# Kernel optimization log

Hardware: AMD Instinct MI355X
Metric: run time of the kernel (lower is better)

The kernel has to match this reference:

```python
import jax, jax.numpy as jnp
import numpy as np

B = 8192      # batch
D = 512       # ode state dim = 4*h_dim
U = 100       # ode net hidden units
K_STEPS = 20  # opt.ode1_step
EPS = 0.01    # opt.ode2_eps


def setup_inputs() -> dict:
    key = jax.random.key(0)
    ks = jax.random.split(key, 12)
    std = 0.1  # init_network_weights std
    return {
        "y0": jax.random.normal(ks[0], (B, D), jnp.float32),
        "t_seq": jax.random.uniform(ks[1], (B, 2), dtype=jnp.float32),
        "W1": std * jax.random.normal(ks[2], (U, D), jnp.float32),
        "b1": jnp.zeros((U,), jnp.float32),
        "W2": std * jax.random.normal(ks[3], (U, U), jnp.float32),
        "b2": jnp.zeros((U,), jnp.float32),
        "W3": std * jax.random.normal(ks[4], (D, U), jnp.float32),
        "b3": jnp.zeros((D,), jnp.float32),
        "b_phi_zt": jax.random.normal(ks[5], (B, 1), jnp.float32),
        # derivative of Nonpositive net is <= 0; log(-b' + 0.01) requires b' < 0.01
        "b_phi_zt_deriv": -jax.random.uniform(ks[6], (B, 1), dtype=jnp.float32),
        "s_phi_zt": jax.random.normal(ks[7], (B, 1), jnp.float32),
        "s_phi_zt_deriv": jax.random.uniform(ks[8], (B, 1), dtype=jnp.float32),
        "k": K_STEPS,
    }


def _ode_net(y, W1, b1, W2, b2, W3, b3):
    # create_net(D, D, n_layers=1, n_units=U): Linear->Tanh->Linear->Tanh->Linear
    h = jnp.tanh(y @ W1.T + b1)
    h = jnp.tanh(h @ W2.T + b2)
    return h @ W3.T + b3


def _forward(y0, t_seq, W1, b1, W2, b2, W3, b3,
             b_phi_zt, b_phi_zt_deriv, s_phi_zt, s_phi_zt_deriv, k):
    # ---- DiffeqSolver: k fixed Euler steps, gradient net ignores t ----
    dt = (t_seq[:, 1:2] - t_seq[:, 0:1]) / k  # [B,1]

    def euler_step(yi, _):
        yi = yi + _ode_net(yi, W1, b1, W2, b2, W3, b3) * dt
        return yi, None

    y_final, _ = jax.lax.scan(euler_step, y0, None, length=k)

    # ---- DiffeqSolver_KL: y_t = y0 + eps * cumsum(g(m_t)); y0 = 0 ----
    const = 0.01
    Kv = s_phi_zt + jnp.log(-b_phi_zt_deriv + const) - jnp.log(s_phi_zt_deriv + const)  # [B,1]
    T = int(round(1.0 / EPS)) - 1  # steps t = 1 .. int(1/eps)-1
    ms = (-1.0 + EPS * jnp.arange(1, T + 1, dtype=jnp.float32))[:, None, None]  # [T,1,1]
    log_neg_m = jnp.log(-ms)
    gm = -b_phi_zt_deriv / (ms * log_neg_m) * (Kv - jnp.log(-log_neg_m))  # [T,B,1]
    ycum = EPS * jnp.cumsum(gm, axis=0)  # solutions[t-1] = ycum[t-1]
    loss = ycum[-1] + (ycum[-2] - ycum[-1])  # first_item + Gm_eps  -> [B,1]

    return jnp.concatenate([y_final, loss], axis=-1)  # [B, D+1]


def reference(y0, t_seq, W1, b1, W2, b2, W3, b3,
              b_phi_zt, b_phi_zt_deriv, s_phi_zt, s_phi_zt_deriv, k):
    return _forward(y0, t_seq, W1, b1, W2, b2, W3, b3,
                    b_phi_zt, b_phi_zt_deriv, s_phi_zt, s_phi_zt_deriv, k)
```

## Files before the change

### kernel.cpp

```cpp
#include <hip/hip_runtime.h>


typedef __attribute__((ext_vector_type(8))) short s16x8;
typedef __attribute__((ext_vector_type(4))) float fx4;

#define NB 8192
#define DD 512
#define UU 100
#define UP 128
#define BM 32
#define YSTR 1040
#define HSTR 272

__device__ __forceinline__ unsigned int f2bf(float x) {
  unsigned int u = __float_as_uint(x);
  return (u + 0x7FFFu + ((u >> 16) & 1u)) >> 16;
}
__device__ __forceinline__ float bf2f(unsigned int h) {
  return __uint_as_float(h << 16);
}
__device__ __forceinline__ unsigned int cvt_pk_bf16(float lo, float hi) {
  unsigned int r;
  asm("v_cvt_pk_bf16_f32 %0, %1, %2" : "=v"(r) : "v"(lo), "v"(hi));
  return r;
}
__device__ __forceinline__ float tanh5(float x) {
  float e = __builtin_amdgcn_exp2f(x * 2.885390081777927f);
  return 1.0f - 2.0f / (e + 1.0f);
}
__device__ __forceinline__ fx4 mfma_a(s16x8 a, s16x8 b, fx4 c) {
  asm("v_mfma_f32_16x16x32_bf16 %0, %1, %2, %0" : "+v"(c) : "a"(a), "v"(b));
  return c;
}

__global__ void prep_weights(const float* __restrict__ W1,
                             const float* __restrict__ W2,
                             const float* __restrict__ W3,
                             const float* __restrict__ b2,
                             const float* __restrict__ b3,
                             unsigned short* __restrict__ ws) {
  int e = blockIdx.x * 256 + threadIdx.x;
  if (e < 65536) {
    int u = e >> 9, kc = e & 511;
    ws[e] = (u < UU) ? (unsigned short)f2bf(W1[u * DD + kc]) : (unsigned short)0;
  } else if (e < 81920) {
    int e2 = e - 65536;
    int n = e2 >> 7, kc = e2 & 127;
    unsigned short v = 0;
    if (kc == 127)      v = (n < UU) ? (unsigned short)f2bf(b2[n]) : (unsigned short)0;
    else if (n < UU && kc < UU) v = (unsigned short)f2bf(W2[n * UU + kc]);
    ws[e] = v;
  } else if (e < 147456) {
    int e3 = e - 81920;
    int d = e3 >> 7, kc = e3 & 127;
    unsigned short v = 0;
    if (kc == 127)      v = (unsigned short)f2bf(b3[d]);
    else if (kc < UU)   v = (unsigned short)f2bf(W3[d * UU + kc]);
    ws[e] = v;
  }
}

__global__ __launch_bounds__(512) __attribute__((amdgpu_waves_per_eu(2, 2)))
void ode_main(
    const float* __restrict__ y0, const float* __restrict__ t_seq,
    const float* __restrict__ b1,
    const unsigned short* __restrict__ W1b,
    const unsigned short* __restrict__ W2b,
    const unsigned short* __restrict__ W3b,
    const int* __restrict__ kptr, float* __restrict__ out) {
  __shared__ char Yb[BM * YSTR];
  __shared__ char H1[BM * HSTR];
  __shared__ char H2[BM * HSTR];

  const int tid  = threadIdx.x;
  const int w    = tid >> 6;
  const int lane = tid & 63;
  const int lo   = lane & 15;
  const int hi   = lane >> 4;
  const int b0   = blockIdx.x * BM;
  const int k    = *kptr;
  const float kinv = 1.0f / (float)k;

  const int yrb  = lo * YSTR + hi * 16;
  const int ywb  = lo * YSTR + w * 128 + hi * 8;
  const int hrb  = lo * HSTR + hi * 16;
  const int hwb  = lo * HSTR + w * 32 + hi * 8;

  s16x8 w1r[16];
#pragma unroll
  for (int kk = 0; kk < 16; ++kk)
    w1r[kk] = *(const s16x8*)(W1b + (16 * w + lo) * DD + kk * 32 + hi * 8);
  s16x8 w2r[4];
#pragma unroll
  for (int kk = 0; kk < 4; ++kk)
    w2r[kk] = *(const s16x8*)(W2b + (16 * w + lo) * UP + kk * 32 + hi * 8);
  s16x8 w3r[4][4];
#pragma unroll
  for (int i = 0; i < 4; ++i)
#pragma unroll
    for (int kk = 0; kk < 4; ++kk)
      w3r[i][kk] = *(const s16x8*)(W3b + ((4 * w + i) * 16 + lo) * UP + kk * 32 + hi * 8);

  float b1v[4];
#pragma unroll
  for (int r = 0; r < 4; ++r) {
    int u = 16 * w + 4 * hi + r;
    b1v[r] = (u < UU) ? b1[u] : 0.0f;
  }
  float dt2[2];
#pragma unroll
  for (int j = 0; j < 2; ++j) {
    int b = b0 + j * 16 + lo;
    dt2[j] = (t_seq[2 * b + 1] - t_seq[2 * b]) * kinv;
  }

  fx4 Yr[4][2];
#pragma unroll
  for (int i = 0; i < 4; ++i)
#pragma unroll
    for (int j = 0; j < 2; ++j) {
      const float* p = y0 + (size_t)(b0 + j * 16 + lo) * DD + (4 * w + i) * 16 + hi * 4;
      Yr[i][j] = *(const fx4*)p;
    }

  auto write_yb = [&]() {
#pragma unroll
    for (int i = 0; i < 4; ++i)
#pragma unroll
      for (int j = 0; j < 2; ++j) {
        uint2 q;
        q.x = cvt_pk_bf16(Yr[i][j][0], Yr[i][j][1]);
        q.y = cvt_pk_bf16(Yr[i][j][2], Yr[i][j][3]);
        *(uint2*)(Yb + ywb + i * 32 + j * 16 * YSTR) = q;
      }
  };
  write_yb();
  __syncthreads();

  const fx4 zf = {0.f, 0.f, 0.f, 0.f};

#pragma unroll 1
  for (int s = 0; s < k; ++s) {
    {
      fx4 aA[2], aB[2];
#pragma unroll
      for (int j = 0; j < 2; ++j)
#pragma unroll
        for (int r = 0; r < 4; ++r) { aA[j][r] = b1v[r]; aB[j][r] = 0.0f; }
      __builtin_amdgcn_s_setprio(1);
#pragma unroll
      for (int kk = 0; kk < 16; kk += 2) {
        s16x8 b00 = *(const s16x8*)(Yb + yrb + kk * 64);
        s16x8 b01 = *(const s16x8*)(Yb + yrb + kk * 64 + 16 * YSTR);
        s16x8 b10 = *(const s16x8*)(Yb + yrb + (kk + 1) * 64);
        s16x8 b11 = *(const s16x8*)(Yb + yrb + (kk + 1) * 64 + 16 * YSTR);
        aA[0] = mfma_a(w1r[kk], b00, aA[0]);
        aA[1] = mfma_a(w1r[kk], b01, aA[1]);
        aB[0] = mfma_a(w1r[kk + 1], b10, aB[0]);
        aB[1] = mfma_a(w1r[kk + 1], b11, aB[1]);
      }
      __builtin_amdgcn_s_setprio(0);
#pragma unroll
      for (int j = 0; j < 2; ++j) {
        float v0 = tanh5(aA[j][0] + aB[j][0]);
        float v1 = tanh5(aA[j][1] + aB[j][1]);
        float v2 = tanh5(aA[j][2] + aB[j][2]);
        float v3 = tanh5(aA[j][3] + aB[j][3]);
        if (w == 7 && hi == 3) v3 = 1.0f;
        uint2 q;
        q.x = cvt_pk_bf16(v0, v1);
        q.y = cvt_pk_bf16(v2, v3);
        *(uint2*)(H1 + hwb + j * 16 * HSTR) = q;
      }
    }
    __syncthreads();

    {
      fx4 c2[2];
      c2[0] = zf; c2[1] = zf;
      __builtin_amdgcn_s_setprio(1);
#pragma unroll
      for (int kk = 0; kk < 4; ++kk) {
        s16x8 hb0 = *(const s16x8*)(H1 + hrb + kk * 64);
        s16x8 hb1 = *(const s16x8*)(H1 + hrb + kk * 64 + 16 * HSTR);
        c2[0] = mfma_a(w2r[kk], hb0, c2[0]);
        c2[1] = mfma_a(w2r[kk], hb1, c2[1]);
      }
      __builtin_amdgcn_s_setprio(0);
#pragma unroll
      for (int j = 0; j < 2; ++j) {
        float h0 = tanh5(c2[j][0]) * dt2[j];
        float h1x = tanh5(c2[j][1]) * dt2[j];
        float h2x = tanh5(c2[j][2]) * dt2[j];
        float h3 = tanh5(c2[j][3]) * dt2[j];
        if (w == 7 && hi == 3) h3 = dt2[j];
        uint2 q;
        q.x = cvt_pk_bf16(h0, h1x);
        q.y = cvt_pk_bf16(h2x, h3);
        *(uint2*)(H2 + hwb + j * 16 * HSTR) = q;
      }
    }
    __syncthreads();

    __builtin_amdgcn_s_setprio(1);
#pragma unroll
    for (int kk = 0; kk < 4; ++kk) {
      s16x8 bb0 = *(const s16x8*)(H2 + hrb + kk * 64);
      s16x8 bb1 = *(const s16x8*)(H2 + hrb + kk * 64 + 16 * HSTR);
#pragma unroll
      for (int i = 0; i < 4; ++i) {
        Yr[i][0] = mfma_a(w3r[i][kk], bb0, Yr[i][0]);
        Yr[i][1] = mfma_a(w3r[i][kk], bb1, Yr[i][1]);
      }
    }
    __builtin_amdgcn_s_setprio(0);
    write_yb();
    __syncthreads();
  }

  for (int idx = tid; idx < BM * DD; idx += 512) {
    int b = idx >> 9, d = idx & 511;
    unsigned short hx = *(const unsigned short*)(Yb + b * YSTR + 2 * d);
    out[(size_t)(b0 + b) * 513 + d] = bf2f((unsigned int)hx);
  }
}

__global__ void loss_kernel(const float* __restrict__ bdp,
                            const float* __restrict__ sp,
                            const float* __restrict__ sdp,
                            float* __restrict__ out) {
  int b = blockIdx.x * 256 + threadIdx.x;
  if (b >= NB) return;
  float bd = bdp[b];
  float Kv = sp[b] + __logf(-bd + 0.01f) - __logf(sdp[b] + 0.01f);
  float acc = 0.0f;
  for (int t = 1; t <= 98; ++t) {
    float m = 0.01f * (float)t - 1.0f;
    float L = __logf(-m);
    acc += (-bd) / (m * L) * (Kv - __logf(-L));
  }
  out[(size_t)b * 513 + 512] = 0.01f * acc;
}

extern "C" void kernel_launch(void* const* d_in, const int* in_sizes, int n_in,
                              void* d_out, int out_size, void* d_ws, size_t ws_size,
                              hipStream_t stream) {
  const float* y0    = (const float*)d_in[0];
  const float* t_seq = (const float*)d_in[1];
  const float* W1    = (const float*)d_in[2];
  const float* b1    = (const float*)d_in[3];
  const float* W2    = (const float*)d_in[4];
  const float* b2    = (const float*)d_in[5];
  const float* W3    = (const float*)d_in[6];
  const float* b3    = (const float*)d_in[7];
  const float* bd    = (const float*)d_in[9];
  const float* s_    = (const float*)d_in[10];
  const float* sd    = (const float*)d_in[11];
  const int*   kptr  = (const int*)d_in[12];
  float* out = (float*)d_out;
  unsigned short* ws = (unsigned short*)d_ws;

  prep_weights<<<576, 256, 0, stream>>>(W1, W2, W3, b2, b3, ws);
  ode_main<<<256, 512, 0, stream>>>(y0, t_seq, b1,
                                    ws, ws + 65536, ws + 81920, kptr, out);
  loss_kernel<<<32, 256, 0, stream>>>(bd, s_, sd, out);
}
```

Before: 93.09 us.

## Use 32x32x16 MFMA with split-K across wave pairs for first ODE layer

Rewrites the first layer GEMM (Y·W1ᵀ) to use 32x32x16 bf16 MFMA instructions. Each wave covers a 32-unit by 32-batch tile over half of the K dimension, and the two halves are reduced through a new shared-memory exchange buffer with an extra barrier. The aim is fewer LDS reads of Y and higher MFMA efficiency per instruction. In exchange it adds an LDS round trip, another __syncthreads per step, and more complex indexing for the bias and H1 writes.

```diff
diff --git a/kernel.cpp b/kernel.cpp
--- a/kernel.cpp
+++ b/kernel.cpp
@@ -3,6 +3,7 @@
 
 typedef __attribute__((ext_vector_type(8))) short s16x8;
 typedef __attribute__((ext_vector_type(4))) float fx4;
+typedef __attribute__((ext_vector_type(16))) float f32x16;
 
 #define NB 8192
 #define DD 512
@@ -11,6 +12,7 @@
 #define BM 32
 #define YSTR 1040
 #define HSTR 272
+#define XSTR 72
 
 __device__ __forceinline__ unsigned int f2bf(float x) {
   unsigned int u = __float_as_uint(x);
@@ -71,25 +73,32 @@
   __shared__ char Yb[BM * YSTR];
   __shared__ char H1[BM * HSTR];
   __shared__ char H2[BM * HSTR];
+  __shared__ char S1x[4 * 64 * XSTR];
 
   const int tid  = threadIdx.x;
   const int w    = tid >> 6;
   const int lane = tid & 63;
   const int lo   = lane & 15;
   const int hi   = lane >> 4;
+  const int c31  = lane & 31;
+  const int h5   = lane >> 5;
+  const int p    = w & 3;
+  const int h    = w >> 2;
   const int b0   = blockIdx.x * BM;
   const int k    = *kptr;
   const float kinv = 1.0f / (float)k;
 
-  const int yrb  = lo * YSTR + hi * 16;
+  const int yrb1 = c31 * YSTR + h * 512 + h5 * 16;
   const int ywb  = lo * YSTR + w * 128 + hi * 8;
   const int hrb  = lo * HSTR + hi * 16;
-  const int hwb  = lo * HSTR + w * 32 + hi * 8;
+  const int hwb2 = lo * HSTR + w * 32 + hi * 8;
+  const int h1wb = c31 * HSTR + p * 64 + h * 32 + h5 * 8;
+  const int xb   = p * (64 * XSTR) + lane * XSTR;
 
   s16x8 w1r[16];
 #pragma unroll
   for (int kk = 0; kk < 16; ++kk)
-    w1r[kk] = *(const s16x8*)(W1b + (16 * w + lo) * DD + kk * 32 + hi * 8);
+    w1r[kk] = *(const s16x8*)(W1b + (p * 32 + c31) * DD + h * 256 + kk * 16 + h5 * 8);
   s16x8 w2r[4];
 #pragma unroll
   for (int kk = 0; kk < 4; ++kk)
@@ -101,12 +110,14 @@
     for (int kk = 0; kk < 4; ++kk)
       w3r[i][kk] = *(const s16x8*)(W3b + ((4 * w + i) * 16 + lo) * UP + kk * 32 + hi * 8);
 
-  float b1v[4];
-#pragma unroll
-  for (int r = 0; r < 4; ++r) {
-    int u = 16 * w + 4 * hi + r;
-    b1v[r] = (u < UU) ? b1[u] : 0.0f;
-  }
+  float b1v[2][4];
+#pragma unroll
+  for (int gg = 0; gg < 2; ++gg)
+#pragma unroll
+    for (int m = 0; m < 4; ++m) {
+      int u = p * 32 + 16 * h + 8 * gg + 4 * h5 + m;
+      b1v[gg][m] = (u < UU) ? b1[u] : 0.0f;
+    }
   float dt2[2];
 #pragma unroll
   for (int j = 0; j < 2; ++j) {
@@ -119,8 +130,8 @@
   for (int i = 0; i < 4; ++i)
 #pragma unroll
     for (int j = 0; j < 2; ++j) {
-      const float* p = y0 + (size_t)(b0 + j * 16 + lo) * DD + (4 * w + i) * 16 + hi * 4;
-      Yr[i][j] = *(const fx4*)p;
+      const float* pp = y0 + (size_t)(b0 + j * 16 + lo) * DD + (4 * w + i) * 16 + hi * 4;
+      Yr[i][j] = *(const fx4*)pp;
     }
 
   auto write_yb = [&]() {
@@ -142,35 +153,44 @@
 #pragma unroll 1
   for (int s = 0; s < k; ++s) {
     {
-      fx4 aA[2], aB[2];
-#pragma unroll
-      for (int j = 0; j < 2; ++j)
-#pragma unroll
-        for (int r = 0; r < 4; ++r) { aA[j][r] = b1v[r]; aB[j][r] = 0.0f; }
+      f32x16 a0, a1;
+#pragma unroll
+      for (int r = 0; r < 16; ++r) { a0[r] = 0.0f; a1[r] = 0.0f; }
       __builtin_amdgcn_s_setprio(1);
 #pragma unroll
       for (int kk = 0; kk < 16; kk += 2) {
-        s16x8 b00 = *(const s16x8*)(Yb + yrb + kk * 64);
-        s16x8 b01 = *(const s16x8*)(Yb + yrb + kk * 64 + 16 * YSTR);
-        s16x8 b10 = *(const s16x8*)(Yb + yrb + (kk + 1) * 64);
-        s16x8 b11 = *(const s16x8*)(Yb + yrb + (kk + 1) * 64 + 16 * YSTR);
-        aA[0] = mfma_a(w1r[kk], b00, aA[0]);
-        aA[1] = mfma_a(w1r[kk], b01, aA[1]);
-        aB[0] = mfma_a(w1r[kk + 1], b10, aB[0]);
-        aB[1] = mfma_a(w1r[kk + 1], b11, aB[1]);
+        s16x8 f0 = *(const s16x8*)(Yb + yrb1 + kk * 32);
+        s16x8 f1 = *(const s16x8*)(Yb + yrb1 + (kk + 1) * 32);
+        a0 = __builtin_amdgcn_mfma_f32_32x32x16_bf16(w1r[kk], f0, a0, 0, 0, 0);
+        a1 = __builtin_amdgcn_mfma_f32_32x32x16_bf16(w1r[kk + 1], f1, a1, 0, 0, 0);
       }
       __builtin_amdgcn_s_setprio(0);
-#pragma unroll
-      for (int j = 0; j < 2; ++j) {
-        float v0 = tanh5(aA[j][0] + aB[j][0]);
-        float v1 = tanh5(aA[j][1] + aB[j][1]);
-        float v2 = tanh5(aA[j][2] + aB[j][2]);
-        float v3 = tanh5(aA[j][3] + aB[j][3]);
-        if (w == 7 && hi == 3) v3 = 1.0f;
+      float sv[8];
+#pragma unroll
+      for (int r = 0; r < 8; ++r) sv[r] = a0[h * 8 + r] + a1[h * 8 + r];
+      fx4 o0, o1;
+#pragma unroll
+      for (int m = 0; m < 4; ++m) {
+        o0[m] = a0[(1 - h) * 8 + m] + a1[(1 - h) * 8 + m];
+        o1[m] = a0[(1 - h) * 8 + 4 + m] + a1[(1 - h) * 8 + 4 + m];
+      }
+      *(fx4*)(S1x + xb + (1 - h) * 32)      = o0;
+      *(fx4*)(S1x + xb + (1 - h) * 32 + 16) = o1;
+      __syncthreads();
+      fx4 p0 = *(const fx4*)(S1x + xb + h * 32);
+      fx4 p1 = *(const fx4*)(S1x + xb + h * 32 + 16);
+#pragma unroll
+      for (int gg = 0; gg < 2; ++gg) {
+        const fx4& pr = gg ? p1 : p0;
+        float v0 = tanh5(sv[4 * gg + 0] + pr[0] + b1v[gg][0]);
+        float v1 = tanh5(sv[4 * gg + 1] + pr[1] + b1v[gg][1]);
+        float v2 = tanh5(sv[4 * gg + 2] + pr[2] + b1v[gg][2]);
+        float v3 = tanh5(sv[4 * gg + 3] + pr[3] + b1v[gg][3]);
+        if (w == 7 && h5 == 1 && gg == 1) v3 = 1.0f;
         uint2 q;
         q.x = cvt_pk_bf16(v0, v1);
         q.y = cvt_pk_bf16(v2, v3);
-        *(uint2*)(H1 + hwb + j * 16 * HSTR) = q;
+        *(uint2*)(H1 + h1wb + gg * 16) = q;
       }
     }
     __syncthreads();
@@ -197,7 +217,7 @@
         uint2 q;
         q.x = cvt_pk_bf16(h0, h1x);
         q.y = cvt_pk_bf16(h2x, h3);
-        *(uint2*)(H2 + hwb + j * 16 * HSTR) = q;
+        *(uint2*)(H2 + hwb2 + j * 16 * HSTR) = q;
       }
     }
     __syncthreads();
```

Result: slower. 153.4 us (+64.8%).

## Split ODE net work across 16 waves with K-split layer-one reduction

Applied to the files above, without the earlier changes.

Doubles the block to 1024 threads (16 waves) and splits layer one along the K dimension into two halves. The two partial sums are exchanged through a new shared scratch buffer and an extra barrier. Layers two and three are divided by batch half and output columns, so each wave holds half the weight registers and half the Y accumulators. The aim is more latency hiding and fewer serial MFMAs per wave, at the cost of an extra sync per step and the LDS partial-sum exchange.

```diff
diff --git a/kernel.cpp b/kernel.cpp
--- a/kernel.cpp
+++ b/kernel.cpp
@@ -11,6 +11,7 @@
 #define BM 32
 #define YSTR 1040
 #define HSTR 272
+#define XSTR 40
 
 __device__ __forceinline__ unsigned int f2bf(float x) {
   unsigned int u = __float_as_uint(x);
@@ -60,7 +61,7 @@
   }
 }
 
-__global__ __launch_bounds__(512) __attribute__((amdgpu_waves_per_eu(2, 2)))
+__global__ __launch_bounds__(1024) __attribute__((amdgpu_waves_per_eu(4, 4)))
 void ode_main(
     const float* __restrict__ y0, const float* __restrict__ t_seq,
     const float* __restrict__ b1,
@@ -71,67 +72,71 @@
   __shared__ char Yb[BM * YSTR];
   __shared__ char H1[BM * HSTR];
   __shared__ char H2[BM * HSTR];
+  __shared__ char S1x[8 * 64 * XSTR];
 
   const int tid  = threadIdx.x;
   const int w    = tid >> 6;
   const int lane = tid & 63;
   const int lo   = lane & 15;
   const int hi   = lane >> 4;
+  const int p    = w & 7;
+  const int h    = w >> 3;
   const int b0   = blockIdx.x * BM;
   const int k    = *kptr;
   const float kinv = 1.0f / (float)k;
 
-  const int yrb  = lo * YSTR + hi * 16;
-  const int ywb  = lo * YSTR + w * 128 + hi * 8;
+  const int yrb  = lo * YSTR + h * 512 + hi * 16;
+  const int ywb  = lo * YSTR + hi * 8;
   const int hrb  = lo * HSTR + hi * 16;
-  const int hwb  = lo * HSTR + w * 32 + hi * 8;
-
-  s16x8 w1r[16];
-#pragma unroll
-  for (int kk = 0; kk < 16; ++kk)
-    w1r[kk] = *(const s16x8*)(W1b + (16 * w + lo) * DD + kk * 32 + hi * 8);
+  const int h1wb = (h * 16 + lo) * HSTR + p * 32 + hi * 8;
+  const int h2wb = (h * 16 + lo) * HSTR + p * 32 + hi * 8;
+  const int xb   = (p * 64 + lane) * XSTR;
+
+  s16x8 w1r[8];
+#pragma unroll
+  for (int kk = 0; kk < 8; ++kk)
+    w1r[kk] = *(const s16x8*)(W1b + (p * 16 + lo) * DD + h * 256 + kk * 32 + hi * 8);
   s16x8 w2r[4];
 #pragma unroll
   for (int kk = 0; kk < 4; ++kk)
-    w2r[kk] = *(const s16x8*)(W2b + (16 * w + lo) * UP + kk * 32 + hi * 8);
-  s16x8 w3r[4][4];
-#pragma unroll
-  for (int i = 0; i < 4; ++i)
+    w2r[kk] = *(const s16x8*)(W2b + (p * 16 + lo) * UP + kk * 32 + hi * 8);
+  s16x8 w3r[2][4];
+#pragma unroll
+  for (int i = 0; i < 2; ++i)
 #pragma unroll
     for (int kk = 0; kk < 4; ++kk)
-      w3r[i][kk] = *(const s16x8*)(W3b + ((4 * w + i) * 16 + lo) * UP + kk * 32 + hi * 8);
+      w3r[i][kk] = *(const s16x8*)(W3b + ((2 * w + i) * 16 + lo) * UP + kk * 32 + hi * 8);
 
   float b1v[4];
 #pragma unroll
   for (int r = 0; r < 4; ++r) {
-    int u = 16 * w + 4 * hi + r;
+    int u = p * 16 + 4 * hi + r;
     b1v[r] = (u < UU) ? b1[u] : 0.0f;
   }
-  float dt2[2];
-#pragma unroll
-  for (int j = 0; j < 2; ++j) {
-    int b = b0 + j * 16 + lo;
-    dt2[j] = (t_seq[2 * b + 1] - t_seq[2 * b]) * kinv;
-  }
-
-  fx4 Yr[4][2];
-#pragma unroll
-  for (int i = 0; i < 4; ++i)
+  float dt2v;
+  {
+    int b = b0 + h * 16 + lo;
+    dt2v = (t_seq[2 * b + 1] - t_seq[2 * b]) * kinv;
+  }
+
+  fx4 Yr[2][2];
+#pragma unroll
+  for (int i = 0; i < 2; ++i)
 #pragma unroll
     for (int j = 0; j < 2; ++j) {
-      const float* p = y0 + (size_t)(b0 + j * 16 + lo) * DD + (4 * w + i) * 16 + hi * 4;
-      Yr[i][j] = *(const fx4*)p;
+      const float* pp = y0 + (size_t)(b0 + j * 16 + lo) * DD + (2 * w + i) * 16 + hi * 4;
+      Yr[i][j] = *(const fx4*)pp;
     }
 
   auto write_yb = [&]() {
 #pragma unroll
-    for (int i = 0; i < 4; ++i)
+    for (int i = 0; i < 2; ++i)
 #pragma unroll
       for (int j = 0; j < 2; ++j) {
         uint2 q;
         q.x = cvt_pk_bf16(Yr[i][j][0], Yr[i][j][1]);
         q.y = cvt_pk_bf16(Yr[i][j][2], Yr[i][j][3]);
-        *(uint2*)(Yb + ywb + i * 32 + j * 16 * YSTR) = q;
+        *(uint2*)(Yb + ywb + j * 16 * YSTR + ((2 * w + i) * 16) * 2) = q;
       }
   };
   write_yb();
@@ -141,64 +146,52 @@
 
 #pragma unroll 1
   for (int s = 0; s < k; ++s) {
+    fx4 a1[2];
+    a1[0] = zf; a1[1] = zf;
+    __builtin_amdgcn_s_setprio(1);
+#pragma unroll
+    for (int kk = 0; kk < 8; ++kk) {
+      s16x8 bb0 = *(const s16x8*)(Yb + yrb + kk * 64);
+      s16x8 bb1 = *(const s16x8*)(Yb + yrb + kk * 64 + 16 * YSTR);
+      a1[0] = mfma_a(w1r[kk], bb0, a1[0]);
+      a1[1] = mfma_a(w1r[kk], bb1, a1[1]);
+    }
+    __builtin_amdgcn_s_setprio(0);
+    *(fx4*)(S1x + xb + (1 - h) * 16) = a1[1 - h];
+    __syncthreads();
+
     {
-      fx4 aA[2], aB[2];
-#pragma unroll
-      for (int j = 0; j < 2; ++j)
-#pragma unroll
-        for (int r = 0; r < 4; ++r) { aA[j][r] = b1v[r]; aB[j][r] = 0.0f; }
+      fx4 pr = *(const fx4*)(S1x + xb + h * 16);
+      float v0 = tanh5(a1[h][0] + pr[0] + b1v[0]);
+      float v1 = tanh5(a1[h][1] + pr[1] + b1v[1]);
+      float v2 = tanh5(a1[h][2] + pr[2] + b1v[2]);
+      float v3 = tanh5(a1[h][3] + pr[3] + b1v[3]);
+      if (p == 7 && hi == 3) v3 = 1.0f;
+      uint2 q;
+      q.x = cvt_pk_bf16(v0, v1);
+      q.y = cvt_pk_bf16(v2, v3);
+      *(uint2*)(H1 + h1wb) = q;
+    }
+    __syncthreads();
+
+    {
+      fx4 c2 = zf;
       __builtin_amdgcn_s_setprio(1);
 #pragma unroll
-      for (int kk = 0; kk < 16; kk += 2) {
-        s16x8 b00 = *(const s16x8*)(Yb + yrb + kk * 64);
-        s16x8 b01 = *(const s16x8*)(Yb + yrb + kk * 64 + 16 * YSTR);
-        s16x8 b10 = *(const s16x8*)(Yb + yrb + (kk + 1) * 64);
-        s16x8 b11 = *(const s16x8*)(Yb + yrb + (kk + 1) * 64 + 16 * YSTR);
-        aA[0] = mfma_a(w1r[kk], b00, aA[0]);
-        aA[1] = mfma_a(w1r[kk], b01, aA[1]);
-        aB[0] = mfma_a(w1r[kk + 1], b10, aB[0]);
-        aB[1] = mfma_a(w1r[kk + 1], b11, aB[1]);
+      for (int kk = 0; kk < 4; ++kk) {
+        s16x8 hb = *(const s16x8*)(H1 + hrb + h * 16 * HSTR + kk * 64);
+        c2 = mfma_a(w2r[kk], hb, c2);
       }
       __builtin_amdgcn_s_setprio(0);
-#pragma unroll
-      for (int j = 0; j < 2; ++j) {
-        float v0 = tanh5(aA[j][0] + aB[j][0]);
-        float v1 = tanh5(aA[j][1] + aB[j][1]);
-        float v2 = tanh5(aA[j][2] + aB[j][2]);
-        float v3 = tanh5(aA[j][3] + aB[j][3]);
-        if (w == 7 && hi == 3) v3 = 1.0f;
-        uint2 q;
-        q.x = cvt_pk_bf16(v0, v1);
-        q.y = cvt_pk_bf16(v2, v3);
-        *(uint2*)(H1 + hwb + j * 16 * HSTR) = q;
-      }
-    }
-    __syncthreads();
-
-    {
-      fx4 c2[2];
-      c2[0] = zf; c2[1] = zf;
-      __builtin_amdgcn_s_setprio(1);
-#pragma unroll
-      for (int kk = 0; kk < 4; ++kk) {
-        s16x8 hb0 = *(const s16x8*)(H1 + hrb + kk * 64);
-        s16x8 hb1 = *(const s16x8*)(H1 + hrb + kk * 64 + 16 * HSTR);
-        c2[0] = mfma_a(w2r[kk], hb0, c2[0]);
-        c2[1] = mfma_a(w2r[kk], hb1, c2[1]);
-      }
-      __builtin_amdgcn_s_setprio(0);
-#pragma unroll
-      for (int j = 0; j < 2; ++j) {
-        float h0 = tanh5(c2[j][0]) * dt2[j];
-        float h1x = tanh5(c2[j][1]) * dt2[j];
-        float h2x = tanh5(c2[j][2]) * dt2[j];
-        float h3 = tanh5(c2[j][3]) * dt2[j];
-        if (w == 7 && hi == 3) h3 = dt2[j];
-        uint2 q;
-        q.x = cvt_pk_bf16(h0, h1x);
-        q.y = cvt_pk_bf16(h2x, h3);
-        *(uint2*)(H2 + hwb + j * 16 * HSTR) = q;
-      }
+      float h0 = tanh5(c2[0]) * dt2v;
+      float h1x = tanh5(c2[1]) * dt2v;
+      float h2x = tanh5(c2[2]) * dt2v;
+      float h3 = tanh5(c2[3]) * dt2v;
+      if (p == 7 && hi == 3) h3 = dt2v;
+      uint2 q;
+      q.x = cvt_pk_bf16(h0, h1x);
+      q.y = cvt_pk_bf16(h2x, h3);
+      *(uint2*)(H2 + h2wb) = q;
     }
     __syncthreads();
 
@@ -208,7 +201,7 @@
       s16x8 bb0 = *(const s16x8*)(H2 + hrb + kk * 64);
       s16x8 bb1 = *(const s16x8*)(H2 + hrb + kk * 64 + 16 * HSTR);
 #pragma unroll
-      for (int i = 0; i < 4; ++i) {
+      for (int i = 0; i < 2; ++i) {
         Yr[i][0] = mfma_a(w3r[i][kk], bb0, Yr[i][0]);
         Yr[i][1] = mfma_a(w3r[i][kk], bb1, Yr[i][1]);
       }
@@ -218,7 +211,7 @@
     __syncthreads();
   }
 
-  for (int idx = tid; idx < BM * DD; idx += 512) {
+  for (int idx = tid; idx < BM * DD; idx += 1024) {
     int b = idx >> 9, d = idx & 511;
     unsigned short hx = *(const unsigned short*)(Yb + b * YSTR + 2 * d);
     out[(size_t)(b0 + b) * 513 + d] = bf2f((unsigned int)hx);
@@ -261,7 +254,7 @@
   unsigned short* ws = (unsigned short*)d_ws;
 
   prep_weights<<<576, 256, 0, stream>>>(W1, W2, W3, b2, b3, ws);
-  ode_main<<<256, 512, 0, stream>>>(y0, t_seq, b1,
-                                    ws, ws + 65536, ws + 81920, kptr, out);
+  ode_main<<<256, 1024, 0, stream>>>(y0, t_seq, b1,
+                                     ws, ws + 65536, ws + 81920, kptr, out);
   loss_kernel<<<32, 256, 0, stream>>>(bd, s_, sd, out);
 }
```

After: 139.3 us. 49.7% more time.
